# Performance work log

Measured on AMD Instinct MI355X. Metric: run time of the kernel, lower is better.

Reference implementation:

```python
import jax, jax.numpy as jnp
import numpy as np

T = 2048          # tokens (prefill, single sequence)
H = 4096          # hidden_size
NH = 32           # num attention heads
NKV = 8           # num kv heads (GQA)
HD = H // NH      # head_dim = 128
EPS = 1e-5
THETA = 10000.0


def setup_inputs() -> dict:
    key = jax.random.key(0)
    k0, k1, k2 = jax.random.split(key, 3)
    return {
        "positions": jnp.arange(T, dtype=jnp.int64 if jax.config.jax_enable_x64 else jnp.int32),
        "hidden_states": jax.random.normal(k0, (T, H), dtype=jnp.float32),
        "w_qkv": jax.random.normal(k1, (H, (NH + 2 * NKV) * HD), dtype=jnp.float32) * 0.02,
        "w_o": jax.random.normal(k2, (NH * HD, H), dtype=jnp.float32) * 0.02,
        "q_norm_w": jnp.ones((NH, HD), dtype=jnp.float32),
        "k_norm_w": jnp.ones((NKV, HD), dtype=jnp.float32),
    }


def _layer_norm(x, w, eps):
    # x: [T, n_heads, HD], w: [n_heads, HD]; mean/var over last dim, fp32 math
    xf = x.astype(jnp.float32)
    mean = xf.mean(-1, keepdims=True)
    var = jnp.square(xf - mean).mean(-1, keepdims=True)
    y = (xf - mean) * jax.lax.rsqrt(var + eps)
    return (w.astype(jnp.float32)[None] * y).astype(x.dtype)


def _rope_interleaved(x, positions):
    # non-neox (GPT-J) style: rotate interleaved pairs. x: [T, n, HD]
    inv_freq = 1.0 / (THETA ** (jnp.arange(0, HD, 2, dtype=jnp.float32) / HD))  # [HD/2]
    freqs = positions.astype(jnp.float32)[:, None] * inv_freq[None, :]          # [T, HD/2]
    cos = jnp.cos(freqs)[:, None, :]  # [T,1,HD/2]
    sin = jnp.sin(freqs)[:, None, :]
    x1 = x[..., 0::2]
    x2 = x[..., 1::2]
    o1 = x1 * cos - x2 * sin
    o2 = x2 * cos + x1 * sin
    return jnp.stack([o1, o2], axis=-1).reshape(x.shape)


def reference(positions, hidden_states, w_qkv, w_o, q_norm_w, k_norm_w):
    qkv = hidden_states @ w_qkv  # [T, (NH+2*NKV)*HD]
    q, k, v = jnp.split(qkv, [NH * HD, (NH + NKV) * HD], axis=-1)
    q = q.reshape(T, NH, HD)
    k = k.reshape(T, NKV, HD)
    v = v.reshape(T, NKV, HD)

    # per-head qk LayerNorm
    q = _layer_norm(q, q_norm_w, EPS)
    k = _layer_norm(k, k_norm_w, EPS)

    # non-neox RoPE
    q = _rope_interleaved(q, positions)
    k = _rope_interleaved(k, positions)

    # GQA: expand kv heads to NH
    rep = NH // NKV
    k = jnp.repeat(k, rep, axis=1)  # [T, NH, HD]
    v = jnp.repeat(v, rep, axis=1)

    scale = HD ** -0.5
    scores = jnp.einsum("qhd,khd->hqk", q * scale, k)  # [NH, T, T]
    causal = jnp.tril(jnp.ones((T, T), dtype=bool))
    scores = jnp.where(causal[None], scores, jnp.finfo(scores.dtype).min)
    probs = jax.nn.softmax(scores, axis=-1)
    attn = jnp.einsum("hqk,khd->qhd", probs, v).reshape(T, NH * HD)

    return attn @ w_o  # [T, H]
```

## Files before the change

kernel.cpp:

```cpp
#include <hip/hip_runtime.h>
#include <cstdint>
#include <cstddef>

#define T_SEQ   2048
#define H_DIM   4096
#define NH_Q    32
#define NKV_H   8
#define HD_     128
#define QKV_N   6144
#define EPS_F   1e-5f
#define ATT_SCALE 0.08838834764831845f
#define LN_THETA  9.210340371976184f

typedef __attribute__((ext_vector_type(8))) short bf16x8;
typedef __attribute__((ext_vector_type(4))) float f32x4;

static __device__ __forceinline__ unsigned short f2bf(float f) {
  union { float f; uint32_t u; } v; v.f = f;
  uint32_t u = v.u;
  u += 0x7fff + ((u >> 16) & 1);
  return (unsigned short)(u >> 16);
}
static __device__ __forceinline__ float bf2f(unsigned short h) {
  union { uint32_t u; float f; } v; v.u = ((uint32_t)h) << 16;
  return v.f;
}

static __device__ __forceinline__ void gld_lds16(const void* g, void* l) {
  __builtin_amdgcn_global_load_lds(
      (const __attribute__((address_space(1))) unsigned int*)g,
      (__attribute__((address_space(3))) unsigned int*)l, 16, 0, 0);
}

__global__ void convert_bf16_kernel(const float* __restrict__ in,
                                    unsigned short* __restrict__ out, int n4) {
  int i = blockIdx.x * blockDim.x + threadIdx.x;
  if (i < n4) {
    float4 f = *(const float4*)(in + (size_t)i * 4);
    ushort4 o;
    o.x = f2bf(f.x); o.y = f2bf(f.y); o.z = f2bf(f.z); o.w = f2bf(f.w);
    *(ushort4*)(out + (size_t)i * 4) = o;
  }
}

__global__ void transpose_bf16_kernel(const float* __restrict__ in,
                                      unsigned short* __restrict__ out,
                                      int R, int C) {
  __shared__ float tile[32][33];
  int c0 = blockIdx.x * 32, r0 = blockIdx.y * 32;
  int tx = threadIdx.x, ty = threadIdx.y;
  for (int i = 0; i < 32; i += 8)
    tile[ty + i][tx] = in[(size_t)(r0 + ty + i) * C + c0 + tx];
  __syncthreads();
  for (int i = 0; i < 32; i += 8)
    out[(size_t)(c0 + ty + i) * R + r0 + tx] = f2bf(tile[tx][ty + i]);
}

template <bool BF16OUT>
__global__ __launch_bounds__(512, 2) void gemm256_kernel(
    const unsigned short* __restrict__ A, const unsigned short* __restrict__ Bt,
    void* __restrict__ Cp, int M, int N, int K) {
  __shared__ unsigned short As[2][256 * 64];
  __shared__ unsigned short Bs[2][256 * 64];
  const int tid = threadIdx.x, lane = tid & 63, wid = tid >> 6;
  const int wm = wid >> 2, wn = wid & 3;
  const int g = lane >> 4, s = lane & 15, s7 = s & 7;
  const int m0 = blockIdx.y * 256, n0 = blockIdx.x * 256;
  const int NT = K >> 6;

  const int lr = lane >> 3, lc = lane & 7;
  const size_t src_lane = (size_t)lr * K + (size_t)((lc ^ lr) * 8);

  auto stage_half = [&](const unsigned short* grow, unsigned short* lhalf) {
    gld_lds16(grow + (size_t)(wid * 16) * K + src_lane, lhalf + wid * 1024);
    gld_lds16(grow + (size_t)(wid * 16 + 8) * K + src_lane,
              lhalf + wid * 1024 + 512);
  };

  const int aroff = (wm * 128 + s) * 64;
  const int broff = (wn * 64 + s) * 64;
  const int ck0 = ((0 * 4 + g) ^ s7) * 8;
  const int ck1 = ((1 * 4 + g) ^ s7) * 8;

  f32x4 acc[8][4] = {};

  stage_half(A  + (size_t)(m0)       * K, &As[0][0]);
  stage_half(A  + (size_t)(m0 + 128) * K, &As[0][128 * 64]);
  stage_half(Bt + (size_t)(n0)       * K, &Bs[0][0]);
  stage_half(Bt + (size_t)(n0 + 128) * K, &Bs[0][128 * 64]);
  stage_half(Bt + (size_t)(n0)       * K + 64, &Bs[1][0]);
  stage_half(Bt + (size_t)(n0 + 128) * K + 64, &Bs[1][128 * 64]);
  asm volatile("s_waitcnt vmcnt(4)" ::: "memory");
  __builtin_amdgcn_s_barrier();

  auto tile_step = [&](unsigned short* cA, unsigned short* cB,
                       unsigned short* nA, int t) {
    const int k0 = t << 6;
    bf16x8 bfr[4][2];
#pragma unroll
    for (int fc = 0; fc < 4; fc++) {
      bfr[fc][0] = *(const bf16x8*)(cB + broff + fc * 1024 + ck0);
      bfr[fc][1] = *(const bf16x8*)(cB + broff + fc * 1024 + ck1);
    }
#pragma unroll
    for (int ph = 0; ph < 4; ph++) {
      bf16x8 a[2][2];
#pragma unroll
      for (int i = 0; i < 2; i++) {
        const int fr = ph * 2 + i;
        a[i][0] = *(const bf16x8*)(cA + aroff + fr * 1024 + ck0);
        a[i][1] = *(const bf16x8*)(cA + aroff + fr * 1024 + ck1);
      }
      if (ph == 0 && t + 1 < NT)
        stage_half(A + (size_t)(m0) * K + k0 + 64, nA);
      if (ph == 1 && t + 1 < NT)
        stage_half(A + (size_t)(m0 + 128) * K + k0 + 64, nA + 128 * 64);
      if (ph == 2 && t + 2 < NT)
        stage_half(Bt + (size_t)(n0) * K + k0 + 128, cB);
      if (ph == 3 && t + 2 < NT)
        stage_half(Bt + (size_t)(n0 + 128) * K + k0 + 128, cB + 128 * 64);
      __builtin_amdgcn_s_barrier();
      asm volatile("s_waitcnt lgkmcnt(0)" ::: "memory");
      __builtin_amdgcn_sched_barrier(0);
      __builtin_amdgcn_s_setprio(1);
#pragma unroll
      for (int i = 0; i < 2; i++) {
        const int fr = ph * 2 + i;
#pragma unroll
        for (int fc = 0; fc < 4; fc++) {
          acc[fr][fc] = __builtin_amdgcn_mfma_f32_16x16x32_bf16(
              a[i][0], bfr[fc][0], acc[fr][fc], 0, 0, 0);
          acc[fr][fc] = __builtin_amdgcn_mfma_f32_16x16x32_bf16(
              a[i][1], bfr[fc][1], acc[fr][fc], 0, 0, 0);
        }
      }
      __builtin_amdgcn_s_setprio(0);
      __builtin_amdgcn_sched_barrier(0);
      if (ph == 3) {
        if (t + 2 < NT) asm volatile("s_waitcnt vmcnt(4)" ::: "memory");
        else            asm volatile("s_waitcnt vmcnt(0)" ::: "memory");
      }
      __builtin_amdgcn_s_barrier();
    }
  };

  for (int t = 0; t < NT; t += 2) {
    tile_step(&As[0][0], &Bs[0][0], &As[1][0], t);
    tile_step(&As[1][0], &Bs[1][0], &As[0][0], t + 1);
  }

#pragma unroll
  for (int fr = 0; fr < 8; fr++)
#pragma unroll
    for (int fc = 0; fc < 4; fc++)
#pragma unroll
      for (int r = 0; r < 4; r++) {
        int m = m0 + wm * 128 + fr * 16 + g * 4 + r;
        int n = n0 + wn * 64 + fc * 16 + s;
        float v = acc[fr][fc][r];
        if (BF16OUT) ((unsigned short*)Cp)[(size_t)m * N + n] = f2bf(v);
        else         ((float*)Cp)[(size_t)m * N + n] = v;
      }
}

__global__ __launch_bounds__(256) void ln_rope_kernel(
    unsigned short* __restrict__ qkv, const int* __restrict__ positions,
    const float* __restrict__ qw, const float* __restrict__ kw) {
  const int wid = threadIdx.x >> 6, lane = threadIdx.x & 63;
  const int rid = blockIdx.x * 4 + wid;
  const int t = rid / 40, hh = rid % 40;
  const bool isq = hh < NH_Q;
  const int col = isq ? hh * HD_ : H_DIM + (hh - NH_Q) * HD_;
  unsigned short* row = qkv + (size_t)t * QKV_N + col;

  uint32_t both = *(const uint32_t*)(row + lane * 2);
  float x1 = bf2f((unsigned short)(both & 0xffff));
  float x2 = bf2f((unsigned short)(both >> 16));
  float ssum = x1 + x2, ssq = x1 * x1 + x2 * x2;
  for (int off = 1; off < 64; off <<= 1) {
    ssum += __shfl_xor(ssum, off, 64);
    ssq  += __shfl_xor(ssq,  off, 64);
  }
  float mean = ssum * (1.0f / HD_);
  float var  = ssq * (1.0f / HD_) - mean * mean;
  float rs = rsqrtf(var + EPS_F);
  const float* w = isq ? (qw + hh * HD_) : (kw + (hh - NH_Q) * HD_);
  float2 wv = *(const float2*)(w + lane * 2);
  float y1 = (x1 - mean) * rs * wv.x;
  float y2 = (x2 - mean) * rs * wv.y;
  float pos = (float)positions[t];
  float inv = __expf(-((float)(2 * lane) * (1.0f / HD_)) * LN_THETA);
  float fr = pos * inv;
  float c = cosf(fr), sn = sinf(fr);
  float o1 = y1 * c - y2 * sn;
  float o2 = y2 * c + y1 * sn;
  if (isq) { o1 *= ATT_SCALE; o2 *= ATT_SCALE; }
  *(uint32_t*)(row + lane * 2) =
      (uint32_t)f2bf(o1) | ((uint32_t)f2bf(o2) << 16);
}

__global__ void vt_kernel(const unsigned short* __restrict__ qkv,
                          unsigned short* __restrict__ vt) {
  __shared__ unsigned short tile[32][33];
  const int kvh = blockIdx.z;
  const int t0 = blockIdx.x * 32, d0 = blockIdx.y * 32;
  const int tx = threadIdx.x, ty = threadIdx.y;
  for (int i = 0; i < 32; i += 8)
    tile[ty + i][tx] =
        qkv[(size_t)(t0 + ty + i) * QKV_N + H_DIM + NKV_H * HD_ + kvh * HD_ + d0 + tx];
  __syncthreads();
  for (int i = 0; i < 32; i += 8)
    vt[((size_t)kvh * HD_ + d0 + ty + i) * T_SEQ + t0 + tx] = tile[tx][ty + i];
}

__global__ __launch_bounds__(256) void attn_kernel(
    const unsigned short* __restrict__ qkv, const unsigned short* __restrict__ vt,
    unsigned short* __restrict__ out) {
  __shared__ unsigned short Ks[64 * 136];
  __shared__ unsigned short Vs[128 * 72];
  __shared__ unsigned short Ps[4][16 * 72];
  const int tid = threadIdx.x, lane = tid & 63, wid = tid >> 6;
  const int g = lane >> 4, s = lane & 15;
  const int h = blockIdx.y;
  const int kvh = h >> 2;
  const int NQT = T_SEQ / 64;

  for (int half = 0; half < 2; half++) {
    const int qt = (half == 0) ? (int)blockIdx.x : NQT - 1 - (int)blockIdx.x;
    const int q0 = qt * 64;

    bf16x8 qf[4];
    {
      const unsigned short* qrow =
          qkv + (size_t)(q0 + wid * 16 + s) * QKV_N + h * HD_;
      for (int ks = 0; ks < 4; ks++)
        qf[ks] = *(const bf16x8*)(qrow + ks * 32 + g * 8);
    }
    f32x4 o[8] = {};
    float m_i[4], l_i[4];
    for (int r = 0; r < 4; r++) { m_i[r] = -1e30f; l_i[r] = 0.f; }

    const int ktiles = qt + 1;
    for (int kt = 0; kt < ktiles; kt++) {
      const int k0 = kt * 64;
      __syncthreads();
      {
        int kr = tid >> 4, kc = tid & 15;
        for (int p = 0; p < 4; p++) {
          bf16x8 v = *(const bf16x8*)(qkv + (size_t)(k0 + kr + p * 16) * QKV_N +
                                      H_DIM + kvh * HD_ + kc * 8);
          *(bf16x8*)&Ks[(kr + p * 16) * 136 + kc * 8] = v;
        }
        int vr = tid >> 3, vc = tid & 7;
        for (int p = 0; p < 4; p++) {
          bf16x8 v = *(const bf16x8*)(vt + ((size_t)kvh * HD_ + vr + p * 32) * T_SEQ +
                                      k0 + vc * 8);
          *(bf16x8*)&Vs[(vr + p * 32) * 72 + vc * 8] = v;
        }
      }
      __syncthreads();
      f32x4 sa[4] = {};
      for (int nt = 0; nt < 4; nt++)
        for (int ks = 0; ks < 4; ks++) {
          bf16x8 kb = *(const bf16x8*)&Ks[(nt * 16 + s) * 136 + ks * 32 + g * 8];
          sa[nt] = __builtin_amdgcn_mfma_f32_16x16x32_bf16(qf[ks], kb, sa[nt], 0, 0, 0);
        }
      if (kt == ktiles - 1) {
        for (int nt = 0; nt < 4; nt++)
          for (int r = 0; r < 4; r++)
            if (k0 + nt * 16 + s > q0 + wid * 16 + g * 4 + r) sa[nt][r] = -1e30f;
      }
      float alpha[4];
      for (int r = 0; r < 4; r++) {
        float mx = fmaxf(fmaxf(sa[0][r], sa[1][r]), fmaxf(sa[2][r], sa[3][r]));
        for (int off = 1; off < 16; off <<= 1) mx = fmaxf(mx, __shfl_xor(mx, off, 64));
        float mn = fmaxf(m_i[r], mx);
        alpha[r] = __expf(m_i[r] - mn);
        m_i[r] = mn;
        float rsum = 0.f;
        for (int nt = 0; nt < 4; nt++) {
          float p = __expf(sa[nt][r] - mn);
          sa[nt][r] = p;
          rsum += p;
        }
        for (int off = 1; off < 16; off <<= 1) rsum += __shfl_xor(rsum, off, 64);
        l_i[r] = l_i[r] * alpha[r] + rsum;
      }
      for (int nt = 0; nt < 4; nt++)
        for (int r = 0; r < 4; r++)
          Ps[wid][(g * 4 + r) * 72 + nt * 16 + s] = f2bf(sa[nt][r]);
      for (int ot = 0; ot < 8; ot++)
        for (int r = 0; r < 4; r++) o[ot][r] *= alpha[r];
      __syncthreads();
      for (int ot = 0; ot < 8; ot++)
        for (int ks = 0; ks < 2; ks++) {
          bf16x8 pa = *(const bf16x8*)&Ps[wid][s * 72 + ks * 32 + g * 8];
          bf16x8 vb = *(const bf16x8*)&Vs[(ot * 16 + s) * 72 + ks * 32 + g * 8];
          o[ot] = __builtin_amdgcn_mfma_f32_16x16x32_bf16(pa, vb, o[ot], 0, 0, 0);
        }
    }
    const size_t obase = (size_t)(q0 + wid * 16);
    for (int ot = 0; ot < 8; ot++)
      for (int r = 0; r < 4; r++) {
        float v = o[ot][r] / l_i[r];
        out[(obase + g * 4 + r) * (size_t)(NH_Q * HD_) + h * HD_ + ot * 16 + s] =
            f2bf(v);
      }
  }
}

extern "C" void kernel_launch(void* const* d_in, const int* in_sizes, int n_in,
                              void* d_out, int out_size, void* d_ws, size_t ws_size,
                              hipStream_t stream) {
  const int*   positions = (const int*)d_in[0];
  const float* hs        = (const float*)d_in[1];
  const float* w_qkv     = (const float*)d_in[2];
  const float* w_o       = (const float*)d_in[3];
  const float* q_norm_w  = (const float*)d_in[4];
  const float* k_norm_w  = (const float*)d_in[5];
  float* out = (float*)d_out;

  char* p = (char*)d_ws;
  unsigned short* hsb   = (unsigned short*)p; p += (size_t)T_SEQ * H_DIM * 2;
  unsigned short* wqkvT = (unsigned short*)p; p += (size_t)QKV_N * H_DIM * 2;
  unsigned short* woT   = (unsigned short*)p; p += (size_t)H_DIM * H_DIM * 2;
  unsigned short* qkvb  = (unsigned short*)p; p += (size_t)T_SEQ * QKV_N * 2;
  unsigned short* attnb = (unsigned short*)p; p += (size_t)T_SEQ * H_DIM * 2;
  unsigned short* vtb   = (unsigned short*)p; p += (size_t)NKV_H * HD_ * T_SEQ * 2;

  convert_bf16_kernel<<<(T_SEQ * H_DIM / 4 + 255) / 256, 256, 0, stream>>>(
      hs, hsb, T_SEQ * H_DIM / 4);
  transpose_bf16_kernel<<<dim3(QKV_N / 32, H_DIM / 32), dim3(32, 8), 0, stream>>>(
      w_qkv, wqkvT, H_DIM, QKV_N);
  transpose_bf16_kernel<<<dim3(H_DIM / 32, H_DIM / 32), dim3(32, 8), 0, stream>>>(
      w_o, woT, H_DIM, H_DIM);
  gemm256_kernel<true><<<dim3(QKV_N / 256, T_SEQ / 256), 512, 0, stream>>>(
      hsb, wqkvT, qkvb, T_SEQ, QKV_N, H_DIM);
  ln_rope_kernel<<<T_SEQ * (NH_Q + NKV_H) / 4, 256, 0, stream>>>(
      qkvb, positions, q_norm_w, k_norm_w);
  vt_kernel<<<dim3(T_SEQ / 32, HD_ / 32, NKV_H), dim3(32, 8), 0, stream>>>(qkvb, vtb);
  attn_kernel<<<dim3(T_SEQ / 128, NH_Q), 256, 0, stream>>>(qkvb, vtb, attnb);
  gemm256_kernel<false><<<dim3(H_DIM / 256, T_SEQ / 256), 512, 0, stream>>>(
      attnb, woT, out, T_SEQ, H_DIM, H_DIM);
}
```

Measured before the change: 600.5 us.

## Templatize GEMM tile width, use narrower N tiles, add setprio in attention

The GEMM kernel now takes its N-tile width (FC*64) and phase count as template parameters. The QKV projection uses 256x192 tiles and the output projection uses 256x128 tiles, which raises the block count to fill more CUs on the 256-CU part. B staging is restructured to match, the lgkmcnt wait and sched barriers are dropped, and the MFMA ordering is split by k-half. The attention kernel also raises wave priority around its MFMA loops. Narrower tiles reuse A less per block and remove explicit LDS waits, so correctness depends on the compiler inserting the needed waits.

```diff
diff --git a/kernel.cpp b/kernel.cpp
--- a/kernel.cpp
+++ b/kernel.cpp
@@ -56,107 +56,129 @@
     out[(size_t)(c0 + ty + i) * R + r0 + tx] = f2bf(tile[tx][ty + i]);
 }
 
-template <bool BF16OUT>
-__global__ __launch_bounds__(512, 2) void gemm256_kernel(
+template <int FC, int PHASES, bool BF16OUT>
+__global__ __launch_bounds__(512) void gemm256_kernel(
     const unsigned short* __restrict__ A, const unsigned short* __restrict__ Bt,
     void* __restrict__ Cp, int M, int N, int K) {
+  constexpr int BN = FC * 64;
+  constexpr int FR_PER = 8 / PHASES;
   __shared__ unsigned short As[2][256 * 64];
-  __shared__ unsigned short Bs[2][256 * 64];
+  __shared__ unsigned short Bs[2][BN * 64];
   const int tid = threadIdx.x, lane = tid & 63, wid = tid >> 6;
   const int wm = wid >> 2, wn = wid & 3;
   const int g = lane >> 4, s = lane & 15, s7 = s & 7;
-  const int m0 = blockIdx.y * 256, n0 = blockIdx.x * 256;
+  const int m0 = blockIdx.y * 256, n0 = blockIdx.x * BN;
   const int NT = K >> 6;
 
   const int lr = lane >> 3, lc = lane & 7;
-  const size_t src_lane = (size_t)lr * K + (size_t)((lc ^ lr) * 8);
-
-  auto stage_half = [&](const unsigned short* grow, unsigned short* lhalf) {
-    gld_lds16(grow + (size_t)(wid * 16) * K + src_lane, lhalf + wid * 1024);
-    gld_lds16(grow + (size_t)(wid * 16 + 8) * K + src_lane,
-              lhalf + wid * 1024 + 512);
+  const size_t srcoff = (size_t)lr * K + (size_t)((lc ^ lr) * 8);
+
+  auto stage_A_half = [&](const unsigned short* gbase, unsigned short* dst,
+                          int h) {
+    const int r0 = wid * 32 + h * 16;
+    gld_lds16(gbase + (size_t)r0 * K + srcoff, dst + r0 * 64);
+    gld_lds16(gbase + (size_t)(r0 + 8) * K + srcoff, dst + (r0 + 8) * 64);
   };
+  auto stage_B = [&](const unsigned short* gbase, unsigned short* dst) {
+#pragma unroll
+    for (int j = 0; j < FC; j++) {
+      const int r0 = wid * (FC * 8) + j * 8;
+      gld_lds16(gbase + (size_t)r0 * K + srcoff, dst + r0 * 64);
+    }
+  };
 
   const int aroff = (wm * 128 + s) * 64;
-  const int broff = (wn * 64 + s) * 64;
+  const int broff = (wn * FC * 16 + s) * 64;
   const int ck0 = ((0 * 4 + g) ^ s7) * 8;
   const int ck1 = ((1 * 4 + g) ^ s7) * 8;
 
-  f32x4 acc[8][4] = {};
-
-  stage_half(A  + (size_t)(m0)       * K, &As[0][0]);
-  stage_half(A  + (size_t)(m0 + 128) * K, &As[0][128 * 64]);
-  stage_half(Bt + (size_t)(n0)       * K, &Bs[0][0]);
-  stage_half(Bt + (size_t)(n0 + 128) * K, &Bs[0][128 * 64]);
-  stage_half(Bt + (size_t)(n0)       * K + 64, &Bs[1][0]);
-  stage_half(Bt + (size_t)(n0 + 128) * K + 64, &Bs[1][128 * 64]);
-  asm volatile("s_waitcnt vmcnt(4)" ::: "memory");
+  f32x4 acc[8][FC] = {};
+
+  stage_A_half(A + (size_t)m0 * K, &As[0][0], 0);
+  stage_A_half(A + (size_t)m0 * K, &As[0][0], 1);
+  stage_B(Bt + (size_t)n0 * K, &Bs[0][0]);
+  stage_B(Bt + (size_t)n0 * K + 64, &Bs[1][0]);
+  if constexpr (FC == 2) asm volatile("s_waitcnt vmcnt(2)" ::: "memory");
+  else                   asm volatile("s_waitcnt vmcnt(3)" ::: "memory");
   __builtin_amdgcn_s_barrier();
 
-  auto tile_step = [&](unsigned short* cA, unsigned short* cB,
-                       unsigned short* nA, int t) {
+  auto tile_step = [&](int t, unsigned short* cA, unsigned short* cB,
+                       unsigned short* nA) {
     const int k0 = t << 6;
-    bf16x8 bfr[4][2];
-#pragma unroll
-    for (int fc = 0; fc < 4; fc++) {
-      bfr[fc][0] = *(const bf16x8*)(cB + broff + fc * 1024 + ck0);
-      bfr[fc][1] = *(const bf16x8*)(cB + broff + fc * 1024 + ck1);
-    }
-#pragma unroll
-    for (int ph = 0; ph < 4; ph++) {
-      bf16x8 a[2][2];
-#pragma unroll
-      for (int i = 0; i < 2; i++) {
-        const int fr = ph * 2 + i;
+    bf16x8 bfr[FC][2];
+#pragma unroll
+    for (int p = 0; p < PHASES; p++) {
+      if (p == 0) {
+#pragma unroll
+        for (int fc = 0; fc < FC; fc++) {
+          bfr[fc][0] = *(const bf16x8*)(cB + broff + fc * 1024 + ck0);
+          bfr[fc][1] = *(const bf16x8*)(cB + broff + fc * 1024 + ck1);
+        }
+      }
+      bf16x8 a[FR_PER][2];
+#pragma unroll
+      for (int i = 0; i < FR_PER; i++) {
+        const int fr = p * FR_PER + i;
         a[i][0] = *(const bf16x8*)(cA + aroff + fr * 1024 + ck0);
         a[i][1] = *(const bf16x8*)(cA + aroff + fr * 1024 + ck1);
       }
-      if (ph == 0 && t + 1 < NT)
-        stage_half(A + (size_t)(m0) * K + k0 + 64, nA);
-      if (ph == 1 && t + 1 < NT)
-        stage_half(A + (size_t)(m0 + 128) * K + k0 + 64, nA + 128 * 64);
-      if (ph == 2 && t + 2 < NT)
-        stage_half(Bt + (size_t)(n0) * K + k0 + 128, cB);
-      if (ph == 3 && t + 2 < NT)
-        stage_half(Bt + (size_t)(n0 + 128) * K + k0 + 128, cB + 128 * 64);
+      if (t + 1 < NT) {
+        if (PHASES == 2) {
+          if (p == 0) {
+            stage_A_half(A + (size_t)m0 * K + k0 + 64, nA, 0);
+            stage_A_half(A + (size_t)m0 * K + k0 + 64, nA, 1);
+          }
+        } else {
+          if (p == 0) stage_A_half(A + (size_t)m0 * K + k0 + 64, nA, 0);
+          if (p == 1) stage_A_half(A + (size_t)m0 * K + k0 + 64, nA, 1);
+        }
+      }
+      if (p == PHASES - 1 && t + 2 < NT)
+        stage_B(Bt + (size_t)n0 * K + k0 + 128, cB);
       __builtin_amdgcn_s_barrier();
-      asm volatile("s_waitcnt lgkmcnt(0)" ::: "memory");
-      __builtin_amdgcn_sched_barrier(0);
       __builtin_amdgcn_s_setprio(1);
 #pragma unroll
-      for (int i = 0; i < 2; i++) {
-        const int fr = ph * 2 + i;
-#pragma unroll
-        for (int fc = 0; fc < 4; fc++) {
+      for (int i = 0; i < FR_PER; i++) {
+        const int fr = p * FR_PER + i;
+#pragma unroll
+        for (int fc = 0; fc < FC; fc++)
           acc[fr][fc] = __builtin_amdgcn_mfma_f32_16x16x32_bf16(
               a[i][0], bfr[fc][0], acc[fr][fc], 0, 0, 0);
+      }
+#pragma unroll
+      for (int i = 0; i < FR_PER; i++) {
+        const int fr = p * FR_PER + i;
+#pragma unroll
+        for (int fc = 0; fc < FC; fc++)
           acc[fr][fc] = __builtin_amdgcn_mfma_f32_16x16x32_bf16(
               a[i][1], bfr[fc][1], acc[fr][fc], 0, 0, 0);
-        }
       }
       __builtin_amdgcn_s_setprio(0);
-      __builtin_amdgcn_sched_barrier(0);
-      if (ph == 3) {
-        if (t + 2 < NT) asm volatile("s_waitcnt vmcnt(4)" ::: "memory");
-        else            asm volatile("s_waitcnt vmcnt(0)" ::: "memory");
+      if (p == PHASES - 1) {
+        if (t + 2 < NT) {
+          if constexpr (FC == 2) asm volatile("s_waitcnt vmcnt(2)" ::: "memory");
+          else                   asm volatile("s_waitcnt vmcnt(3)" ::: "memory");
+        } else {
+          asm volatile("s_waitcnt vmcnt(0)" ::: "memory");
+        }
       }
       __builtin_amdgcn_s_barrier();
     }
   };
 
   for (int t = 0; t < NT; t += 2) {
-    tile_step(&As[0][0], &Bs[0][0], &As[1][0], t);
-    tile_step(&As[1][0], &Bs[1][0], &As[0][0], t + 1);
+    tile_step(t,     &As[0][0], &Bs[0][0], &As[1][0]);
+    tile_step(t + 1, &As[1][0], &Bs[1][0], &As[0][0]);
   }
 
 #pragma unroll
   for (int fr = 0; fr < 8; fr++)
 #pragma unroll
-    for (int fc = 0; fc < 4; fc++)
+    for (int fc = 0; fc < FC; fc++)
 #pragma unroll
       for (int r = 0; r < 4; r++) {
         int m = m0 + wm * 128 + fr * 16 + g * 4 + r;
-        int n = n0 + wn * 64 + fc * 16 + s;
+        int n = n0 + wn * FC * 16 + fc * 16 + s;
         float v = acc[fr][fc][r];
         if (BF16OUT) ((unsigned short*)Cp)[(size_t)m * N + n] = f2bf(v);
         else         ((float*)Cp)[(size_t)m * N + n] = v;
@@ -260,11 +282,13 @@
       }
       __syncthreads();
       f32x4 sa[4] = {};
+      __builtin_amdgcn_s_setprio(1);
       for (int nt = 0; nt < 4; nt++)
         for (int ks = 0; ks < 4; ks++) {
           bf16x8 kb = *(const bf16x8*)&Ks[(nt * 16 + s) * 136 + ks * 32 + g * 8];
           sa[nt] = __builtin_amdgcn_mfma_f32_16x16x32_bf16(qf[ks], kb, sa[nt], 0, 0, 0);
         }
+      __builtin_amdgcn_s_setprio(0);
       if (kt == ktiles - 1) {
         for (int nt = 0; nt < 4; nt++)
           for (int r = 0; r < 4; r++)
@@ -292,12 +316,14 @@
       for (int ot = 0; ot < 8; ot++)
         for (int r = 0; r < 4; r++) o[ot][r] *= alpha[r];
       __syncthreads();
+      __builtin_amdgcn_s_setprio(1);
       for (int ot = 0; ot < 8; ot++)
         for (int ks = 0; ks < 2; ks++) {
           bf16x8 pa = *(const bf16x8*)&Ps[wid][s * 72 + ks * 32 + g * 8];
           bf16x8 vb = *(const bf16x8*)&Vs[(ot * 16 + s) * 72 + ks * 32 + g * 8];
           o[ot] = __builtin_amdgcn_mfma_f32_16x16x32_bf16(pa, vb, o[ot], 0, 0, 0);
         }
+      __builtin_amdgcn_s_setprio(0);
     }
     const size_t obase = (size_t)(q0 + wid * 16);
     for (int ot = 0; ot < 8; ot++)
@@ -334,12 +360,12 @@
       w_qkv, wqkvT, H_DIM, QKV_N);
   transpose_bf16_kernel<<<dim3(H_DIM / 32, H_DIM / 32), dim3(32, 8), 0, stream>>>(
       w_o, woT, H_DIM, H_DIM);
-  gemm256_kernel<true><<<dim3(QKV_N / 256, T_SEQ / 256), 512, 0, stream>>>(
+  gemm256_kernel<3, 4, true><<<dim3(QKV_N / 192, T_SEQ / 256), 512, 0, stream>>>(
       hsb, wqkvT, qkvb, T_SEQ, QKV_N, H_DIM);
   ln_rope_kernel<<<T_SEQ * (NH_Q + NKV_H) / 4, 256, 0, stream>>>(
       qkvb, positions, q_norm_w, k_norm_w);
   vt_kernel<<<dim3(T_SEQ / 32, HD_ / 32, NKV_H), dim3(32, 8), 0, stream>>>(qkvb, vtb);
   attn_kernel<<<dim3(T_SEQ / 128, NH_Q), 256, 0, stream>>>(qkvb, vtb, attnb);
-  gemm256_kernel<false><<<dim3(H_DIM / 256, T_SEQ / 256), 512, 0, stream>>>(
+  gemm256_kernel<2, 2, false><<<dim3(H_DIM / 128, T_SEQ / 256), 512, 0, stream>>>(
       attnb, woT, out, T_SEQ, H_DIM, H_DIM);
 }
```

Result: faster. 566.0 us (-5.7%).

## Split-K the output projection GEMM and retune MFMA scheduling priorities

Applied to the files above, without the earlier changes.

The output projection GEMM now splits K in two across blockIdx.z, doubling the block count from 128 to 256 so more CUs are busy. The second half writes fp32 partials into the reused wqkvT workspace, and a new elementwise kernel adds them into the output. The GEMM inner loop also drops the explicit lgkmcnt wait and sched barriers, reorders the MFMAs by k-half, and removes the occupancy hint from launch bounds. The attention kernel raises wave priority around its MFMA blocks. In exchange the change adds an extra fp32 read and write pass over the output and gives the compiler more scheduling freedom.

```diff
diff --git a/kernel.cpp b/kernel.cpp
--- a/kernel.cpp
+++ b/kernel.cpp
@@ -57,23 +57,28 @@
 }
 
 template <bool BF16OUT>
-__global__ __launch_bounds__(512, 2) void gemm256_kernel(
+__global__ __launch_bounds__(512) void gemm256_kernel(
     const unsigned short* __restrict__ A, const unsigned short* __restrict__ Bt,
-    void* __restrict__ Cp, int M, int N, int K) {
+    void* __restrict__ C0, void* __restrict__ C1,
+    int M, int N, int Ks, int Kl) {
   __shared__ unsigned short As[2][256 * 64];
   __shared__ unsigned short Bs[2][256 * 64];
   const int tid = threadIdx.x, lane = tid & 63, wid = tid >> 6;
   const int wm = wid >> 2, wn = wid & 3;
   const int g = lane >> 4, s = lane & 15, s7 = s & 7;
   const int m0 = blockIdx.y * 256, n0 = blockIdx.x * 256;
-  const int NT = K >> 6;
+  const int z = blockIdx.z;
+  const unsigned short* Ab = A + (size_t)z * Kl;
+  const unsigned short* Bb = Bt + (size_t)z * Kl;
+  void* Cp = z ? C1 : C0;
+  const int NT = Kl >> 6;
 
   const int lr = lane >> 3, lc = lane & 7;
-  const size_t src_lane = (size_t)lr * K + (size_t)((lc ^ lr) * 8);
+  const size_t srcoff = (size_t)lr * Ks + (size_t)((lc ^ lr) * 8);
 
   auto stage_half = [&](const unsigned short* grow, unsigned short* lhalf) {
-    gld_lds16(grow + (size_t)(wid * 16) * K + src_lane, lhalf + wid * 1024);
-    gld_lds16(grow + (size_t)(wid * 16 + 8) * K + src_lane,
+    gld_lds16(grow + (size_t)(wid * 16) * Ks + srcoff, lhalf + wid * 1024);
+    gld_lds16(grow + (size_t)(wid * 16 + 8) * Ks + srcoff,
               lhalf + wid * 1024 + 512);
   };
 
@@ -84,12 +89,12 @@
 
   f32x4 acc[8][4] = {};
 
-  stage_half(A  + (size_t)(m0)       * K, &As[0][0]);
-  stage_half(A  + (size_t)(m0 + 128) * K, &As[0][128 * 64]);
-  stage_half(Bt + (size_t)(n0)       * K, &Bs[0][0]);
-  stage_half(Bt + (size_t)(n0 + 128) * K, &Bs[0][128 * 64]);
-  stage_half(Bt + (size_t)(n0)       * K + 64, &Bs[1][0]);
-  stage_half(Bt + (size_t)(n0 + 128) * K + 64, &Bs[1][128 * 64]);
+  stage_half(Ab + (size_t)(m0)       * Ks, &As[0][0]);
+  stage_half(Ab + (size_t)(m0 + 128) * Ks, &As[0][128 * 64]);
+  stage_half(Bb + (size_t)(n0)       * Ks, &Bs[0][0]);
+  stage_half(Bb + (size_t)(n0 + 128) * Ks, &Bs[0][128 * 64]);
+  stage_half(Bb + (size_t)(n0)       * Ks + 64, &Bs[1][0]);
+  stage_half(Bb + (size_t)(n0 + 128) * Ks + 64, &Bs[1][128 * 64]);
   asm volatile("s_waitcnt vmcnt(4)" ::: "memory");
   __builtin_amdgcn_s_barrier();
 
@@ -112,30 +117,32 @@
         a[i][1] = *(const bf16x8*)(cA + aroff + fr * 1024 + ck1);
       }
       if (ph == 0 && t + 1 < NT)
-        stage_half(A + (size_t)(m0) * K + k0 + 64, nA);
+        stage_half(Ab + (size_t)(m0) * Ks + k0 + 64, nA);
       if (ph == 1 && t + 1 < NT)
-        stage_half(A + (size_t)(m0 + 128) * K + k0 + 64, nA + 128 * 64);
+        stage_half(Ab + (size_t)(m0 + 128) * Ks + k0 + 64, nA + 128 * 64);
       if (ph == 2 && t + 2 < NT)
-        stage_half(Bt + (size_t)(n0) * K + k0 + 128, cB);
+        stage_half(Bb + (size_t)(n0) * Ks + k0 + 128, cB);
       if (ph == 3 && t + 2 < NT)
-        stage_half(Bt + (size_t)(n0 + 128) * K + k0 + 128, cB + 128 * 64);
+        stage_half(Bb + (size_t)(n0 + 128) * Ks + k0 + 128, cB + 128 * 64);
       __builtin_amdgcn_s_barrier();
-      asm volatile("s_waitcnt lgkmcnt(0)" ::: "memory");
-      __builtin_amdgcn_sched_barrier(0);
       __builtin_amdgcn_s_setprio(1);
 #pragma unroll
       for (int i = 0; i < 2; i++) {
         const int fr = ph * 2 + i;
 #pragma unroll
-        for (int fc = 0; fc < 4; fc++) {
+        for (int fc = 0; fc < 4; fc++)
           acc[fr][fc] = __builtin_amdgcn_mfma_f32_16x16x32_bf16(
               a[i][0], bfr[fc][0], acc[fr][fc], 0, 0, 0);
+      }
+#pragma unroll
+      for (int i = 0; i < 2; i++) {
+        const int fr = ph * 2 + i;
+#pragma unroll
+        for (int fc = 0; fc < 4; fc++)
           acc[fr][fc] = __builtin_amdgcn_mfma_f32_16x16x32_bf16(
               a[i][1], bfr[fc][1], acc[fr][fc], 0, 0, 0);
-        }
       }
       __builtin_amdgcn_s_setprio(0);
-      __builtin_amdgcn_sched_barrier(0);
       if (ph == 3) {
         if (t + 2 < NT) asm volatile("s_waitcnt vmcnt(4)" ::: "memory");
         else            asm volatile("s_waitcnt vmcnt(0)" ::: "memory");
@@ -161,6 +168,17 @@
         if (BF16OUT) ((unsigned short*)Cp)[(size_t)m * N + n] = f2bf(v);
         else         ((float*)Cp)[(size_t)m * N + n] = v;
       }
+}
+
+__global__ void addf_kernel(float* __restrict__ o, const float* __restrict__ p,
+                            int n4) {
+  int i = blockIdx.x * blockDim.x + threadIdx.x;
+  if (i < n4) {
+    float4 a = *(const float4*)(o + (size_t)i * 4);
+    float4 b = *(const float4*)(p + (size_t)i * 4);
+    a.x += b.x; a.y += b.y; a.z += b.z; a.w += b.w;
+    *(float4*)(o + (size_t)i * 4) = a;
+  }
 }
 
 __global__ __launch_bounds__(256) void ln_rope_kernel(
@@ -260,11 +278,13 @@
       }
       __syncthreads();
       f32x4 sa[4] = {};
+      __builtin_amdgcn_s_setprio(1);
       for (int nt = 0; nt < 4; nt++)
         for (int ks = 0; ks < 4; ks++) {
           bf16x8 kb = *(const bf16x8*)&Ks[(nt * 16 + s) * 136 + ks * 32 + g * 8];
           sa[nt] = __builtin_amdgcn_mfma_f32_16x16x32_bf16(qf[ks], kb, sa[nt], 0, 0, 0);
         }
+      __builtin_amdgcn_s_setprio(0);
       if (kt == ktiles - 1) {
         for (int nt = 0; nt < 4; nt++)
           for (int r = 0; r < 4; r++)
@@ -292,12 +312,14 @@
       for (int ot = 0; ot < 8; ot++)
         for (int r = 0; r < 4; r++) o[ot][r] *= alpha[r];
       __syncthreads();
+      __builtin_amdgcn_s_setprio(1);
       for (int ot = 0; ot < 8; ot++)
         for (int ks = 0; ks < 2; ks++) {
           bf16x8 pa = *(const bf16x8*)&Ps[wid][s * 72 + ks * 32 + g * 8];
           bf16x8 vb = *(const bf16x8*)&Vs[(ot * 16 + s) * 72 + ks * 32 + g * 8];
           o[ot] = __builtin_amdgcn_mfma_f32_16x16x32_bf16(pa, vb, o[ot], 0, 0, 0);
         }
+      __builtin_amdgcn_s_setprio(0);
     }
     const size_t obase = (size_t)(q0 + wid * 16);
     for (int ot = 0; ot < 8; ot++)
@@ -327,6 +349,7 @@
   unsigned short* qkvb  = (unsigned short*)p; p += (size_t)T_SEQ * QKV_N * 2;
   unsigned short* attnb = (unsigned short*)p; p += (size_t)T_SEQ * H_DIM * 2;
   unsigned short* vtb   = (unsigned short*)p; p += (size_t)NKV_H * HD_ * T_SEQ * 2;
+  float* part1 = (float*)wqkvT;
 
   convert_bf16_kernel<<<(T_SEQ * H_DIM / 4 + 255) / 256, 256, 0, stream>>>(
       hs, hsb, T_SEQ * H_DIM / 4);
@@ -334,12 +357,14 @@
       w_qkv, wqkvT, H_DIM, QKV_N);
   transpose_bf16_kernel<<<dim3(H_DIM / 32, H_DIM / 32), dim3(32, 8), 0, stream>>>(
       w_o, woT, H_DIM, H_DIM);
-  gemm256_kernel<true><<<dim3(QKV_N / 256, T_SEQ / 256), 512, 0, stream>>>(
-      hsb, wqkvT, qkvb, T_SEQ, QKV_N, H_DIM);
+  gemm256_kernel<true><<<dim3(QKV_N / 256, T_SEQ / 256, 1), 512, 0, stream>>>(
+      hsb, wqkvT, qkvb, nullptr, T_SEQ, QKV_N, H_DIM, H_DIM);
   ln_rope_kernel<<<T_SEQ * (NH_Q + NKV_H) / 4, 256, 0, stream>>>(
       qkvb, positions, q_norm_w, k_norm_w);
   vt_kernel<<<dim3(T_SEQ / 32, HD_ / 32, NKV_H), dim3(32, 8), 0, stream>>>(qkvb, vtb);
   attn_kernel<<<dim3(T_SEQ / 128, NH_Q), 256, 0, stream>>>(qkvb, vtb, attnb);
-  gemm256_kernel<false><<<dim3(H_DIM / 256, T_SEQ / 256), 512, 0, stream>>>(
-      attnb, woT, out, T_SEQ, H_DIM, H_DIM);
-}
+  gemm256_kernel<false><<<dim3(H_DIM / 256, T_SEQ / 256, 2), 512, 0, stream>>>(
+      attnb, woT, out, part1, T_SEQ, H_DIM, H_DIM, H_DIM / 2);
+  addf_kernel<<<(T_SEQ * H_DIM / 4 + 255) / 256, 256, 0, stream>>>(
+      out, part1, T_SEQ * H_DIM / 4);
+}
```

Result: faster. 571.3 us (-4.9%).
